# Kernel tuning notes

Measured on AMD Instinct MI355X. Metric: run time of the kernel, lower is better.

Reference implementation:

```python
import jax, jax.numpy as jnp
import numpy as np

N = 50000
E = 800000
IN_DIM = 64
HID = 64
OUT = 40


def setup_inputs() -> dict:
    key = jax.random.key(0)
    ks = jax.random.split(key, 10)
    x = jax.random.normal(ks[0], (N, IN_DIM), dtype=jnp.float32)
    edge_index = jax.random.randint(ks[1], (2, E), 0, N, dtype=jnp.int64)

    def lin(k, fan_in, fan_out):
        # torch nn.Linear default init: U(-1/sqrt(fan_in), 1/sqrt(fan_in))
        bound = 1.0 / np.sqrt(fan_in)
        kw, kb = jax.random.split(k)
        W = jax.random.uniform(kw, (fan_in, fan_out), minval=-bound, maxval=bound, dtype=jnp.float32)
        b = jax.random.uniform(kb, (fan_out,), minval=-bound, maxval=bound, dtype=jnp.float32)
        return W, b

    W1, b1 = lin(ks[2], IN_DIM, HID)   # conv layer 1
    W2, b2 = lin(ks[3], HID, HID)      # conv layer 2
    Wp1, bp1 = lin(ks[4], HID, HID)    # post_mp linear 1
    Wp2, bp2 = lin(ks[5], HID, OUT)    # post_mp linear 2
    return {"x": x, "edge_index": edge_index,
            "W1": W1, "b1": b1, "W2": W2, "b2": b2,
            "Wp1": Wp1, "bp1": bp1, "Wp2": Wp2, "bp2": bp2}


def _mean_aggregate(h, src, dst, num_nodes):
    # Row-normalized sparse adjacency matmul: out[i] = (1/deg(i)) * sum_{(i,j) in E} h[j]
    # adj[src, dst] = 1/deg(src), where deg(src) = #outgoing edges of src.
    ones = jnp.ones((src.shape[0],), dtype=h.dtype)
    deg = jax.ops.segment_sum(ones, src, num_segments=num_nodes)
    w = 1.0 / deg[src]                         # [E], every src has deg >= 1
    msgs = h[dst] * w[:, None]                 # [E, d] gather + scale
    return jax.ops.segment_sum(msgs, src, num_segments=num_nodes)  # [N, d]


def reference(x, edge_index, W1, b1, W2, b2, Wp1, bp1, Wp2, bp2):
    src = edge_index[0]
    dst = edge_index[1]
    n = x.shape[0]
    # GraphSAGEConvolution layer 1: (dropout=eval noop) linear -> spmm mean-agg -> relu
    h = x @ W1 + b1
    h = _mean_aggregate(h, src, dst, n)
    h = jax.nn.relu(h)
    # GraphSAGEConvolution layer 2
    h = h @ W2 + b2
    h = _mean_aggregate(h, src, dst, n)
    h = jax.nn.relu(h)
    # post_mp: Linear -> (dropout noop) -> Linear
    h = h @ Wp1 + bp1
    h = h @ Wp2 + bp2
    return jax.nn.log_softmax(h, axis=1)
```

## Files before the change

kernel.cpp:

```cpp
#include <hip/hip_runtime.h>
#include <cmath>


typedef _Float16 half_t;
typedef half_t half2_t __attribute__((ext_vector_type(2)));
typedef half_t half4_t __attribute__((ext_vector_type(4)));

#if defined(__has_builtin)
# if __has_builtin(__builtin_amdgcn_fdot2)
#  define FDOT2(a, b, c) __builtin_amdgcn_fdot2((a), (b), (c), false)
# endif
#endif
#ifndef FDOT2
# define FDOT2(a, b, c) fmaf((float)(a)[0], (float)(b)[0], fmaf((float)(a)[1], (float)(b)[1], (c)))
#endif

#define NXCD 8
#define CAP  64
#define EDGE_BLOCKS 1024
#define WS 66

__global__ __launch_bounds__(256) void build_h1(
    const int* __restrict__ src, const int* __restrict__ dst,
    const float* __restrict__ x, const float* __restrict__ W1,
    const float* __restrict__ b1,
    const float* __restrict__ W2, const float* __restrict__ Wp1,
    const float* __restrict__ Wp2,
    half_t* __restrict__ Wt, int* __restrict__ cnt,
    unsigned short* __restrict__ col, half_t* __restrict__ Hh,
    int E, int N)
{
    const int tid = threadIdx.x;

    if (blockIdx.x < EDGE_BLOCKS) {
        int gid = blockIdx.x * 256 + tid;
        if (gid < 3 * 4096) {
            int which = gid >> 12, r = gid & 4095;
            int c = r >> 6, k = r & 63;
            float v;
            if      (which == 0) v = W2[k * 64 + c];
            else if (which == 1) v = Wp1[k * 64 + c];
            else                 v = (c < 40) ? Wp2[k * 40 + c] : 0.f;
            Wt[gid] = (half_t)v;
        }

        const int g     = blockIdx.x & (NXCD - 1);
        const int bpg   = blockIdx.x >> 3;
        const int nbpg  = EDGE_BLOCKS >> 3;
        const int chunk = (N + NXCD - 1) / NXCD;
        const int lo = g * chunk;
        const int hi = min(N, lo + chunk);
        const int4* src4 = (const int4*)src;
        const int quads = E >> 2;
        for (int q = bpg * 256 + tid; q < quads; q += nbpg * 256) {
            int4 s4 = src4[q];
            int e = q * 4;
            if (s4.x >= lo && s4.x < hi) {
                int pos = atomicAdd(&cnt[s4.x], 1);
                if (pos < CAP) col[(size_t)s4.x * CAP + pos] = (unsigned short)dst[e + 0];
            }
            if (s4.y >= lo && s4.y < hi) {
                int pos = atomicAdd(&cnt[s4.y], 1);
                if (pos < CAP) col[(size_t)s4.y * CAP + pos] = (unsigned short)dst[e + 1];
            }
            if (s4.z >= lo && s4.z < hi) {
                int pos = atomicAdd(&cnt[s4.z], 1);
                if (pos < CAP) col[(size_t)s4.z * CAP + pos] = (unsigned short)dst[e + 2];
            }
            if (s4.w >= lo && s4.w < hi) {
                int pos = atomicAdd(&cnt[s4.w], 1);
                if (pos < CAP) col[(size_t)s4.w * CAP + pos] = (unsigned short)dst[e + 3];
            }
        }
        if (blockIdx.x == 0 && tid < (E & 3)) {
            int e = (E & ~3) + tid;
            int s = src[e];
            int pos = atomicAdd(&cnt[s], 1);
            if (pos < CAP) col[(size_t)s * CAP + pos] = (unsigned short)dst[e];
        }
    } else {
        __shared__ half_t xs[16][64];
        const int lane = tid & 63;
        const int wid  = tid >> 6;
        const int row0 = (blockIdx.x - EDGE_BLOCKS) * 16;

        for (int i = tid; i < 16 * 64; i += 256) {
            int rr = row0 + (i >> 6);
            float v = (rr < N) ? x[(size_t)row0 * 64 + i] : 0.f;
            xs[i >> 6][i & 63] = (half_t)v;
        }
        const float bias = b1[lane];
        __syncthreads();

        float acc[4] = {bias, bias, bias, bias};
#pragma unroll 1
        for (int c = 0; c < 4; ++c) {
            half2_t wr[8];
#pragma unroll
            for (int j = 0; j < 8; ++j) {
                float a0 = W1[(c * 16 + 2 * j + 0) * 64 + lane];
                float a1 = W1[(c * 16 + 2 * j + 1) * 64 + lane];
                half2_t h; h[0] = (half_t)a0; h[1] = (half_t)a1;
                wr[j] = h;
            }
#pragma unroll
            for (int r = 0; r < 4; ++r) {
                const half2_t* xp = (const half2_t*)&xs[wid * 4 + r][c * 16];
#pragma unroll
                for (int j = 0; j < 8; ++j) acc[r] = FDOT2(xp[j], wr[j], acc[r]);
            }
        }
#pragma unroll
        for (int r = 0; r < 4; ++r) {
            int grow = row0 + wid * 4 + r;
            if (grow < N) Hh[(size_t)grow * 64 + lane] = (half_t)acc[r];
        }
    }
}

__device__ __forceinline__ void gather_node(const half_t* __restrict__ H,
                                            const unsigned short* __restrict__ cbase,
                                            int deg, int grp, int sub, float* f) {
    const half4_t* __restrict__ H4 = (const half4_t*)H;
    const int myt = (int)cbase[threadIdx.x & 63];
    f[0] = f[1] = f[2] = f[3] = 0.f;
    const int full = deg & ~15;
    int e = 0;
    for (; e < full; e += 16) {
        half4_t hacc; hacc[0] = (half_t)0.f; hacc[1] = (half_t)0.f;
        hacc[2] = (half_t)0.f; hacc[3] = (half_t)0.f;
#pragma unroll
        for (int i = 0; i < 4; ++i) {
            int t = __shfl(myt, e + 4 * i + grp);
            hacc += H4[(size_t)t * 16 + sub];
        }
        f[0] += (float)hacc[0]; f[1] += (float)hacc[1];
        f[2] += (float)hacc[2]; f[3] += (float)hacc[3];
    }
    if (e < deg) {
        half4_t hacc; hacc[0] = (half_t)0.f; hacc[1] = (half_t)0.f;
        hacc[2] = (half_t)0.f; hacc[3] = (half_t)0.f;
#pragma unroll
        for (int i = 0; i < 4; ++i) {
            int idx = e + 4 * i + grp;
            int t = __shfl(myt, idx & 63);
            if (idx < deg) hacc += H4[(size_t)t * 16 + sub];
        }
        f[0] += (float)hacc[0]; f[1] += (float)hacc[1];
        f[2] += (float)hacc[2]; f[3] += (float)hacc[3];
    }
#pragma unroll
    for (int k = 0; k < 4; ++k) {
        f[k] += __shfl_xor(f[k], 16);
        f[k] += __shfl_xor(f[k], 32);
    }
}

__device__ __forceinline__ void stage_w(const half_t* __restrict__ Wt,
                                        half_t* __restrict__ wlds, int tid, int nthr) {
    const unsigned* ws = (const unsigned*)Wt;
    unsigned* wd = (unsigned*)wlds;
    for (int i = tid; i < 2048; i += nthr) {
        int c = i >> 5, kp = i & 31;
        wd[c * (WS / 2) + kp] = ws[i];
    }
}

__global__ __launch_bounds__(512) void fused_gather_gemm(
    const half_t* __restrict__ H, const int* __restrict__ cnt,
    const unsigned short* __restrict__ colb, const half_t* __restrict__ Wt,
    const float* __restrict__ b, half_t* __restrict__ Y, int N)
{
    __shared__ half_t wlds[64 * WS];
    __shared__ __align__(16) half_t xrow[8][64];
    const int tid  = threadIdx.x;
    const int w    = tid >> 6;
    const int lane = tid & 63;
    const int grp  = lane >> 4;
    const int sub  = lane & 15;

    stage_w(Wt, wlds, tid, 512);
    __syncthreads();

    const int node = blockIdx.x * 8 + w;
    if (node >= N) return;

    const int deg = cnt[node];
    float f[4];
    gather_node(H, colb + (size_t)node * CAP, deg, grp, sub, f);
    if (grp == 0) {
        float inv = (deg > 0) ? 1.f / (float)deg : 0.f;
        half4_t o;
        o[0] = (half_t)fmaxf(f[0] * inv, 0.f);
        o[1] = (half_t)fmaxf(f[1] * inv, 0.f);
        o[2] = (half_t)fmaxf(f[2] * inv, 0.f);
        o[3] = (half_t)fmaxf(f[3] * inv, 0.f);
        ((half4_t*)xrow[w])[sub] = o;
    }

    float a0 = b[lane], a1 = 0.f;
    const half2_t* wl = (const half2_t*)(wlds + (size_t)lane * WS);
    const half2_t* xp = (const half2_t*)xrow[w];
#pragma unroll
    for (int i = 0; i < 16; ++i) {
        a0 = FDOT2(xp[2 * i + 0], wl[2 * i + 0], a0);
        a1 = FDOT2(xp[2 * i + 1], wl[2 * i + 1], a1);
    }
    Y[(size_t)node * 64 + lane] = (half_t)(a0 + a1);
}

__global__ __launch_bounds__(256) void gemm40_softmax(const half_t* __restrict__ H3,
                                                      const half_t* __restrict__ Wt2,
                                                      const float* __restrict__ bp2,
                                                      float* __restrict__ out, int n) {
    __shared__ half_t xs[16][64];
    const int tid  = threadIdx.x;
    const int lane = tid & 63;
    const int wid  = tid >> 6;
    const int row0 = blockIdx.x * 16;

    {
        const half2_t* X2 = (const half2_t*)H3;
        half2_t z; z[0] = (half_t)0.f; z[1] = (half_t)0.f;
        for (int i = tid; i < 16 * 32; i += 256) {
            int rr = row0 + (i >> 5);
            ((half2_t*)xs)[i] = (rr < n) ? X2[(size_t)row0 * 32 + i] : z;
        }
    }
    const float bias2 = (lane < 40) ? bp2[lane] : 0.f;
    __syncthreads();

    float acc[4] = {bias2, bias2, bias2, bias2};
    const half2_t* wcol = (const half2_t*)(Wt2 + (size_t)lane * 64);
#pragma unroll
    for (int c = 0; c < 4; ++c) {
        half2_t wr[8];
#pragma unroll
        for (int i = 0; i < 8; ++i) wr[i] = wcol[c * 8 + i];
#pragma unroll
        for (int r = 0; r < 4; ++r) {
            const half2_t* xp = (const half2_t*)&xs[wid * 4 + r][c * 16];
#pragma unroll
            for (int i = 0; i < 8; ++i) acc[r] = FDOT2(xp[i], wr[i], acc[r]);
        }
    }

#pragma unroll
    for (int r = 0; r < 4; ++r) {
        float vm = (lane < 40) ? acc[r] : -INFINITY;
        float m = vm;
#pragma unroll
        for (int o = 32; o; o >>= 1) m = fmaxf(m, __shfl_xor(m, o));
        float e = (lane < 40) ? expf(vm - m) : 0.f;
        float s = e;
#pragma unroll
        for (int o = 32; o; o >>= 1) s += __shfl_xor(s, o);
        float ls = logf(s);
        const int grow = row0 + wid * 4 + r;
        if (grow < n && lane < 40) out[(size_t)grow * 40 + lane] = vm - m - ls;
    }
}

extern "C" void kernel_launch(void* const* d_in, const int* in_sizes, int n_in,
                              void* d_out, int out_size, void* d_ws, size_t ws_size,
                              hipStream_t stream) {
    const float* x   = (const float*)d_in[0];
    const int*   ei  = (const int*)d_in[1];
    const float* W1  = (const float*)d_in[2];
    const float* b1  = (const float*)d_in[3];
    const float* W2  = (const float*)d_in[4];
    const float* b2  = (const float*)d_in[5];
    const float* Wp1 = (const float*)d_in[6];
    const float* bp1 = (const float*)d_in[7];
    const float* Wp2 = (const float*)d_in[8];
    const float* bp2 = (const float*)d_in[9];
    float* out = (float*)d_out;

    const int N = in_sizes[0] / 64;
    const int E = in_sizes[1] / 2;
    const int* src = ei;
    const int* dst = ei + E;

    char*  wsb = (char*)d_ws;
    size_t off = 0;
    auto alloc = [&](size_t bytes) { void* p = wsb + off; off += (bytes + 511) & ~(size_t)511; return p; };
    int*            cnt = (int*)alloc((size_t)N * 4);
    unsigned short* col = (unsigned short*)alloc((size_t)N * CAP * 2);
    half_t*         Wt  = (half_t*)alloc((size_t)3 * 4096 * 2);
    half_t*         Ha  = (half_t*)alloc((size_t)N * 64 * 2);
    half_t*         Hb  = (half_t*)alloc((size_t)N * 64 * 2);
    (void)ws_size; (void)n_in; (void)out_size;

    const int nb16 = (N + 15) / 16;
    const int nb8  = (N + 7) / 8;

    hipMemsetAsync(cnt, 0, (size_t)N * 4, stream);
    build_h1<<<EDGE_BLOCKS + nb16, 256, 0, stream>>>(src, dst, x, W1, b1, W2, Wp1, Wp2,
                                                     Wt, cnt, col, Ha, E, N);
    fused_gather_gemm<<<nb8, 512, 0, stream>>>(Ha, cnt, col, Wt + 0 * 4096, b2, Hb, N);
    fused_gather_gemm<<<nb8, 512, 0, stream>>>(Hb, cnt, col, Wt + 1 * 4096, bp1, Ha, N);
    gemm40_softmax<<<nb16, 256, 0, stream>>>(Ha, Wt + 2 * 4096, bp2, out, N);
}
```

Baseline: 135.4 us.

## Skip dst loads for off-partition edges, precompute byte offsets, stage Wp2 in LDS

Result: no change. 135.3 us (-0.1%).

```diff
diff --git a/kernel.cpp b/kernel.cpp
--- a/kernel.cpp
+++ b/kernel.cpp
@@ -51,25 +51,29 @@
         const int lo = g * chunk;
         const int hi = min(N, lo + chunk);
         const int4* src4 = (const int4*)src;
+        const int4* dst4 = (const int4*)dst;
         const int quads = E >> 2;
         for (int q = bpg * 256 + tid; q < quads; q += nbpg * 256) {
             int4 s4 = src4[q];
-            int e = q * 4;
+            bool any = (s4.x >= lo && s4.x < hi) || (s4.y >= lo && s4.y < hi) ||
+                       (s4.z >= lo && s4.z < hi) || (s4.w >= lo && s4.w < hi);
+            if (!any) continue;
+            int4 d4 = dst4[q];
             if (s4.x >= lo && s4.x < hi) {
                 int pos = atomicAdd(&cnt[s4.x], 1);
-                if (pos < CAP) col[(size_t)s4.x * CAP + pos] = (unsigned short)dst[e + 0];
+                if (pos < CAP) col[(size_t)s4.x * CAP + pos] = (unsigned short)d4.x;
             }
             if (s4.y >= lo && s4.y < hi) {
                 int pos = atomicAdd(&cnt[s4.y], 1);
-                if (pos < CAP) col[(size_t)s4.y * CAP + pos] = (unsigned short)dst[e + 1];
+                if (pos < CAP) col[(size_t)s4.y * CAP + pos] = (unsigned short)d4.y;
             }
             if (s4.z >= lo && s4.z < hi) {
                 int pos = atomicAdd(&cnt[s4.z], 1);
-                if (pos < CAP) col[(size_t)s4.z * CAP + pos] = (unsigned short)dst[e + 2];
+                if (pos < CAP) col[(size_t)s4.z * CAP + pos] = (unsigned short)d4.z;
             }
             if (s4.w >= lo && s4.w < hi) {
                 int pos = atomicAdd(&cnt[s4.w], 1);
-                if (pos < CAP) col[(size_t)s4.w * CAP + pos] = (unsigned short)dst[e + 3];
+                if (pos < CAP) col[(size_t)s4.w * CAP + pos] = (unsigned short)d4.w;
             }
         }
         if (blockIdx.x == 0 && tid < (E & 3)) {
@@ -118,11 +122,10 @@
     }
 }
 
-__device__ __forceinline__ void gather_node(const half_t* __restrict__ H,
+__device__ __forceinline__ void gather_node(const char* __restrict__ Hbytes,
                                             const unsigned short* __restrict__ cbase,
-                                            int deg, int grp, int sub, float* f) {
-    const half4_t* __restrict__ H4 = (const half4_t*)H;
-    const int myt = (int)cbase[threadIdx.x & 63];
+                                            int deg, int grp, int suboff, float* f) {
+    const int myo = ((int)cbase[threadIdx.x & 63]) << 7;
     f[0] = f[1] = f[2] = f[3] = 0.f;
     const int full = deg & ~15;
     int e = 0;
@@ -131,8 +134,8 @@
         hacc[2] = (half_t)0.f; hacc[3] = (half_t)0.f;
 #pragma unroll
         for (int i = 0; i < 4; ++i) {
-            int t = __shfl(myt, e + 4 * i + grp);
-            hacc += H4[(size_t)t * 16 + sub];
+            int off = __shfl(myo, e + 4 * i + grp);
+            hacc += *(const half4_t*)(Hbytes + off + suboff);
         }
         f[0] += (float)hacc[0]; f[1] += (float)hacc[1];
         f[2] += (float)hacc[2]; f[3] += (float)hacc[3];
@@ -143,8 +146,8 @@
 #pragma unroll
         for (int i = 0; i < 4; ++i) {
             int idx = e + 4 * i + grp;
-            int t = __shfl(myt, idx & 63);
-            if (idx < deg) hacc += H4[(size_t)t * 16 + sub];
+            int off = __shfl(myo, idx & 63);
+            if (idx < deg) hacc += *(const half4_t*)(Hbytes + off + suboff);
         }
         f[0] += (float)hacc[0]; f[1] += (float)hacc[1];
         f[2] += (float)hacc[2]; f[3] += (float)hacc[3];
@@ -187,7 +190,7 @@
 
     const int deg = cnt[node];
     float f[4];
-    gather_node(H, colb + (size_t)node * CAP, deg, grp, sub, f);
+    gather_node((const char*)H, colb + (size_t)node * CAP, deg, grp, sub * 8, f);
     if (grp == 0) {
         float inv = (deg > 0) ? 1.f / (float)deg : 0.f;
         half4_t o;
@@ -214,11 +217,13 @@
                                                       const float* __restrict__ bp2,
                                                       float* __restrict__ out, int n) {
     __shared__ half_t xs[16][64];
+    __shared__ half_t wlds[64 * WS];
     const int tid  = threadIdx.x;
     const int lane = tid & 63;
     const int wid  = tid >> 6;
     const int row0 = blockIdx.x * 16;
 
+    stage_w(Wt2, wlds, tid, 256);
     {
         const half2_t* X2 = (const half2_t*)H3;
         half2_t z; z[0] = (half_t)0.f; z[1] = (half_t)0.f;
@@ -231,17 +236,17 @@
     __syncthreads();
 
     float acc[4] = {bias2, bias2, bias2, bias2};
-    const half2_t* wcol = (const half2_t*)(Wt2 + (size_t)lane * 64);
-#pragma unroll
-    for (int c = 0; c < 4; ++c) {
-        half2_t wr[8];
-#pragma unroll
-        for (int i = 0; i < 8; ++i) wr[i] = wcol[c * 8 + i];
+    const half2_t* wl = (const half2_t*)(wlds + (size_t)lane * WS);
+#pragma unroll
+    for (int c = 0; c < 2; ++c) {
+        half2_t wr[16];
+#pragma unroll
+        for (int i = 0; i < 16; ++i) wr[i] = wl[c * 16 + i];
 #pragma unroll
         for (int r = 0; r < 4; ++r) {
-            const half2_t* xp = (const half2_t*)&xs[wid * 4 + r][c * 16];
-#pragma unroll
-            for (int i = 0; i < 8; ++i) acc[r] = FDOT2(xp[i], wr[i], acc[r]);
+            const half2_t* xp = (const half2_t*)&xs[wid * 4 + r][c * 32];
+#pragma unroll
+            for (int i = 0; i < 16; ++i) acc[r] = FDOT2(xp[i], wr[i], acc[r]);
         }
     }
 
```
